# Optimization experiments

Measured on AMD Instinct MI355X. Metric: run time of the kernel, lower is better.

Reference implementation:

```python
import jax, jax.numpy as jnp
import numpy as np

N, E, L, S = 10000, 200000, 128, 10
NODE_IN, EDGE_IN = 29, 4  # vel_hist(15)+vel_mag(5)+bound(6)+force(3); rel_disp(3)+rel_dist(1)
EPS = 1e-5  # haiku LayerNorm default


def _mlp(x, params):
    # hk.nets.MLP([L]*num_mlp_layers + [out]) with relu activations
    for W, b in params[:-1]:
        x = jax.nn.relu(x @ W + b)
    W, b = params[-1]
    return x @ W + b


def _ln(x, s, o):
    m = jnp.mean(x, axis=-1, keepdims=True)
    v = jnp.mean(jnp.square(x - m), axis=-1, keepdims=True)
    return (x - m) * jax.lax.rsqrt(v + EPS) * s + o


def _init_mlp(key, dims, stack=None):
    Ws, bs = [], []
    for i in range(len(dims) - 1):
        key, k = jax.random.split(key)
        shp = (dims[i], dims[i + 1]) if stack is None else (stack, dims[i], dims[i + 1])
        Ws.append(jax.random.normal(k, shp, jnp.float32) / np.float32(np.sqrt(dims[i])))
        bshp = (dims[i + 1],) if stack is None else (stack, dims[i + 1])
        bs.append(jnp.zeros(bshp, jnp.float32))
    return Ws, bs


def setup_inputs() -> dict:
    key = jax.random.key(0)
    ks = jax.random.split(key, 16)
    inp = {
        'vel_hist': jax.random.normal(ks[0], (N, 15), jnp.float32),
        'vel_mag': jax.random.normal(ks[1], (N, 5), jnp.float32),
        'bound': jax.random.normal(ks[2], (N, 6), jnp.float32),
        'force': jax.random.normal(ks[3], (N, 3), jnp.float32),
        'rel_disp': jax.random.normal(ks[4], (E, 3), jnp.float32),
        'rel_dist': jax.random.normal(ks[5], (E, 1), jnp.float32),
        'senders': jax.random.randint(ks[6], (E,), 0, N, jnp.int32),
        'receivers': jax.random.randint(ks[7], (E,), 0, N, jnp.int32),
    }
    enW, enB = _init_mlp(ks[8], [NODE_IN, L, L, L])
    eeW, eeB = _init_mlp(ks[9], [EDGE_IN, L, L, L])
    peW, peB = _init_mlp(ks[10], [3 * L, L, L, L], stack=S)
    pnW, pnB = _init_mlp(ks[11], [2 * L, L, L, L], stack=S)
    deW, deB = _init_mlp(ks[12], [L, L, L, 3])
    for pre, (Ws, Bs) in [('en', (enW, enB)), ('ee', (eeW, eeB)), ('pe', (peW, peB)), ('pn', (pnW, pnB)), ('de', (deW, deB))]:
        for i in range(3):
            inp[f'{pre}_W{i}'] = Ws[i]
            inp[f'{pre}_b{i}'] = Bs[i]
    inp['en_s'] = jnp.ones((L,), jnp.float32); inp['en_o'] = jnp.zeros((L,), jnp.float32)
    inp['ee_s'] = jnp.ones((L,), jnp.float32); inp['ee_o'] = jnp.zeros((L,), jnp.float32)
    inp['pe_s'] = jnp.ones((S, L), jnp.float32); inp['pe_o'] = jnp.zeros((S, L), jnp.float32)
    inp['pn_s'] = jnp.ones((S, L), jnp.float32); inp['pn_o'] = jnp.zeros((S, L), jnp.float32)
    return inp


def reference(vel_hist, vel_mag, bound, force, rel_disp, rel_dist,
              en_W0, en_b0, en_W1, en_b1, en_W2, en_b2, en_s, en_o,
              ee_W0, ee_b0, ee_W1, ee_b1, ee_W2, ee_b2, ee_s, ee_o,
              pe_W0, pe_b0, pe_W1, pe_b1, pe_W2, pe_b2, pe_s, pe_o,
              pn_W0, pn_b0, pn_W1, pn_b1, pn_W2, pn_b2, pn_s, pn_o,
              de_W0, de_b0, de_W1, de_b1, de_W2, de_b2,
              senders, receivers):
    n = vel_hist.shape[0]
    # encoder
    nodes = _ln(_mlp(jnp.concatenate([vel_hist, vel_mag, bound, force], -1),
                     [(en_W0, en_b0), (en_W1, en_b1), (en_W2, en_b2)]), en_s, en_o)
    edges = _ln(_mlp(jnp.concatenate([rel_disp, rel_dist], -1),
                     [(ee_W0, ee_b0), (ee_W1, ee_b1), (ee_W2, ee_b2)]), ee_s, ee_o)

    # processor: S GraphNetwork blocks with residual adds (distinct params per step)
    def step(carry, p):
        nd, ed = carry
        (W0, b0, W1, b1, W2, b2, s, o, nW0, nb0, nW1, nb1, nW2, nb2, ns, no) = p
        e_in = jnp.concatenate([nd[senders], nd[receivers], ed], -1)  # [E, 3L]
        e_new = _ln(_mlp(e_in, [(W0, b0), (W1, b1), (W2, b2)]), s, o)
        aggr = jax.ops.segment_sum(e_new, receivers, num_segments=n)  # [N, L]
        n_new = _ln(_mlp(jnp.concatenate([nd, aggr], -1), [(nW0, nb0), (nW1, nb1), (nW2, nb2)]), ns, no)
        return (nd + n_new, ed + e_new), None

    (nodes, edges), _ = jax.lax.scan(
        step, (nodes, edges),
        (pe_W0, pe_b0, pe_W1, pe_b1, pe_W2, pe_b2, pe_s, pe_o,
         pn_W0, pn_b0, pn_W1, pn_b1, pn_W2, pn_b2, pn_s, pn_o))

    # decoder (no layer norm)
    return _mlp(nodes, [(de_W0, de_b0), (de_W1, de_b1), (de_W2, de_b2)])
```

## Files before the change

kernel.cpp:

```cpp
#include <hip/hip_runtime.h>

#define NN 10000
#define NE 200000
#define LDIM 128
#define PADB 136
#define NSTEP 10
#define LN_EPS 1e-5f

typedef unsigned short ushort_t;
typedef __attribute__((ext_vector_type(8))) short short8;
typedef __attribute__((ext_vector_type(4))) float f32x4;

#define MFMA16(a, b, c) __builtin_amdgcn_mfma_f32_16x16x32_bf16(a, b, c, 0, 0, 0)

__device__ __forceinline__ ushort_t f2bf(float f) {
  unsigned int u = __float_as_uint(f);
  return (ushort_t)((u + 0x7FFFu + ((u >> 16) & 1u)) >> 16);
}
__device__ __forceinline__ float bf2f(ushort_t h) {
  return __uint_as_float(((unsigned int)h) << 16);
}

#define STAGE_WT(WT, KTOT, K0)                                              \
  {                                                                         \
    const ushort_t* src_ = (WT) + (size_t)(t >> 1) * (KTOT) + (K0) + (t & 1) * 64; \
    ushort_t* dst_ = &Wbuf[(t >> 1) * PADB + (t & 1) * 64];                 \
    _Pragma("unroll")                                                       \
    for (int q_ = 0; q_ < 8; ++q_)                                          \
      *(uint4*)(dst_ + q_ * 8) = *(const uint4*)(src_ + q_ * 8);            \
  }

#define INIT_ACC(BG)                                                        \
  _Pragma("unroll")                                                         \
  for (int nt_ = 0; nt_ < 8; ++nt_) {                                       \
    float bv_ = (BG)[nt_ * 16 + lr];                                        \
    acc[0][nt_] = (f32x4){bv_, bv_, bv_, bv_};                              \
    acc[1][nt_] = acc[0][nt_];                                              \
  }

#define MFMA_K128()                                                         \
  _Pragma("unroll")                                                         \
  for (int ks_ = 0; ks_ < 4; ++ks_) {                                       \
    short8 a0_ = *(const short8*)&Abuf[(rw + lr) * PADB + ks_ * 32 + kg * 8];        \
    short8 a1_ = *(const short8*)&Abuf[(rw + 16 + lr) * PADB + ks_ * 32 + kg * 8];   \
    _Pragma("unroll")                                                       \
    for (int nt_ = 0; nt_ < 8; ++nt_) {                                     \
      short8 b_ = *(const short8*)&Wbuf[(nt_ * 16 + lr) * PADB + ks_ * 32 + kg * 8]; \
      acc[0][nt_] = MFMA16(a0_, b_, acc[0][nt_]);                           \
      acc[1][nt_] = MFMA16(a1_, b_, acc[1][nt_]);                           \
    }                                                                       \
  }

#define RELU_TO_ABUF()                                                      \
  _Pragma("unroll")                                                         \
  for (int mt_ = 0; mt_ < 2; ++mt_) {                                       \
    _Pragma("unroll")                                                       \
    for (int nt_ = 0; nt_ < 8; ++nt_) {                                     \
      _Pragma("unroll")                                                     \
      for (int i_ = 0; i_ < 4; ++i_) {                                      \
        int row_ = rw + 16 * mt_ + kg * 4 + i_;                             \
        Abuf[row_ * PADB + nt_ * 16 + lr] = f2bf(fmaxf(acc[mt_][nt_][i_], 0.f)); \
      }                                                                     \
    }                                                                       \
  }

#define LN_STATS2(MARR, RARR)                                               \
  float MARR[2][4], RARR[2][4];                                             \
  _Pragma("unroll")                                                         \
  for (int mt_ = 0; mt_ < 2; ++mt_) {                                       \
    _Pragma("unroll")                                                       \
    for (int i_ = 0; i_ < 4; ++i_) {                                        \
      float s_ = 0.f;                                                       \
      _Pragma("unroll")                                                     \
      for (int nt_ = 0; nt_ < 8; ++nt_) s_ += acc[mt_][nt_][i_];            \
      s_ += __shfl_xor(s_, 1); s_ += __shfl_xor(s_, 2);                     \
      s_ += __shfl_xor(s_, 4); s_ += __shfl_xor(s_, 8);                     \
      float m_ = s_ * (1.f / 128.f);                                        \
      float v_ = 0.f;                                                       \
      _Pragma("unroll")                                                     \
      for (int nt_ = 0; nt_ < 8; ++nt_) {                                   \
        float d_ = acc[mt_][nt_][i_] - m_; v_ = fmaf(d_, d_, v_);           \
      }                                                                     \
      v_ += __shfl_xor(v_, 1); v_ += __shfl_xor(v_, 2);                     \
      v_ += __shfl_xor(v_, 4); v_ += __shfl_xor(v_, 8);                     \
      MARR[mt_][i_] = m_;                                                   \
      RARR[mt_][i_] = rsqrtf(v_ * (1.f / 128.f) + LN_EPS);                  \
    }                                                                       \
  }

#define INIT_ACC1(BG)                                                       \
  _Pragma("unroll")                                                         \
  for (int nt_ = 0; nt_ < 8; ++nt_) {                                       \
    float bv_ = (BG)[nt_ * 16 + lr];                                        \
    acc[nt_] = (f32x4){bv_, bv_, bv_, bv_};                                 \
  }

#define MFMA_K128_M16()                                                     \
  _Pragma("unroll")                                                         \
  for (int ks_ = 0; ks_ < 4; ++ks_) {                                       \
    short8 a_ = *(const short8*)&Abuf[(rw + lr) * PADB + ks_ * 32 + kg * 8];         \
    _Pragma("unroll")                                                       \
    for (int nt_ = 0; nt_ < 8; ++nt_) {                                     \
      short8 b_ = *(const short8*)&Wbuf[(nt_ * 16 + lr) * PADB + ks_ * 32 + kg * 8]; \
      acc[nt_] = MFMA16(a_, b_, acc[nt_]);                                  \
    }                                                                       \
  }

#define RELU_TO_ABUF1()                                                     \
  _Pragma("unroll")                                                         \
  for (int nt_ = 0; nt_ < 8; ++nt_) {                                       \
    _Pragma("unroll")                                                       \
    for (int i_ = 0; i_ < 4; ++i_) {                                        \
      int row_ = rw + kg * 4 + i_;                                          \
      Abuf[row_ * PADB + nt_ * 16 + lr] = f2bf(fmaxf(acc[nt_][i_], 0.f));   \
    }                                                                       \
  }

#define LN_STATS1(MARR, RARR)                                               \
  float MARR[4], RARR[4];                                                   \
  _Pragma("unroll")                                                         \
  for (int i_ = 0; i_ < 4; ++i_) {                                          \
    float s_ = 0.f;                                                         \
    _Pragma("unroll")                                                       \
    for (int nt_ = 0; nt_ < 8; ++nt_) s_ += acc[nt_][i_];                   \
    s_ += __shfl_xor(s_, 1); s_ += __shfl_xor(s_, 2);                       \
    s_ += __shfl_xor(s_, 4); s_ += __shfl_xor(s_, 8);                       \
    float m_ = s_ * (1.f / 128.f);                                          \
    float v_ = 0.f;                                                         \
    _Pragma("unroll")                                                       \
    for (int nt_ = 0; nt_ < 8; ++nt_) {                                     \
      float d_ = acc[nt_][i_] - m_; v_ = fmaf(d_, d_, v_);                  \
    }                                                                       \
    v_ += __shfl_xor(v_, 1); v_ += __shfl_xor(v_, 2);                       \
    v_ += __shfl_xor(v_, 4); v_ += __shfl_xor(v_, 8);                       \
    MARR[i_] = m_;                                                          \
    RARR[i_] = rsqrtf(v_ * (1.f / 128.f) + LN_EPS);                         \
  }

#define STAGE_WT512(WT, KTOT, K0)                                           \
  {                                                                         \
    const ushort_t* src_ = (WT) + (size_t)(t >> 2) * (KTOT) + (K0) + (t & 3) * 32; \
    ushort_t* dst_ = &Wbuf[(t >> 2) * PADB + (t & 3) * 32];                 \
    _Pragma("unroll")                                                       \
    for (int q_ = 0; q_ < 4; ++q_)                                          \
      *(uint4*)(dst_ + q_ * 8) = *(const uint4*)(src_ + q_ * 8);            \
  }

__global__ void k_prep_w(const float* __restrict__ src, ushort_t* __restrict__ dst,
                         int Ksrc, int Kdst, int N, int steps) {
  const size_t total = (size_t)steps * N * Kdst;
  for (size_t idx = (size_t)blockIdx.x * blockDim.x + threadIdx.x; idx < total;
       idx += (size_t)gridDim.x * blockDim.x) {
    int k = (int)(idx % Kdst);
    size_t tmp = idx / Kdst;
    int n = (int)(tmp % N);
    int s = (int)(tmp / N);
    float v = (k < Ksrc) ? src[((size_t)s * Ksrc + k) * N + n] : 0.f;
    dst[idx] = f2bf(v);
  }
}

__global__ void k_hist(const int* __restrict__ recv, int* __restrict__ cnt) {
  int e = blockIdx.x * 256 + threadIdx.x;
  if (e < NE) atomicAdd(&cnt[recv[e]], 1);
}

__global__ __launch_bounds__(256)
void k_scan(const int* __restrict__ cnt, int* __restrict__ row_start) {
  __shared__ int part[256];
  const int t = threadIdx.x;
  const int base = t * 40;
  int sum = 0;
  for (int i = 0; i < 40; ++i) {
    int b = base + i;
    if (b < NN) sum += cnt[b];
  }
  part[t] = sum;
  __syncthreads();
  for (int off = 1; off < 256; off <<= 1) {
    int v = part[t];
    int u = (t >= off) ? part[t - off] : 0;
    __syncthreads();
    part[t] = v + u;
    __syncthreads();
  }
  int run = (t == 0) ? 0 : part[t - 1];
  for (int i = 0; i < 40; ++i) {
    int b = base + i;
    if (b < NN) { row_start[b] = run; run += cnt[b]; }
  }
  if (t == 255) row_start[NN] = run;
}

__global__ void k_scatter(const int* __restrict__ send, const int* __restrict__ recv,
                          const int* __restrict__ row_start, int* __restrict__ cursor,
                          int* __restrict__ esrc, int* __restrict__ sSend,
                          int* __restrict__ sRecv) {
  int e = blockIdx.x * 256 + threadIdx.x;
  if (e >= NE) return;
  int r = recv[e];
  int pos = row_start[r] + atomicAdd(&cursor[r], 1);
  esrc[pos] = e;
  sSend[pos] = send[e];
  sRecv[pos] = r;
}

__global__ __launch_bounds__(256, 2)
void k_enc_node_m(const float* __restrict__ vh, const float* __restrict__ vm,
                  const float* __restrict__ bd, const float* __restrict__ fc,
                  const ushort_t* __restrict__ Wt0, const float* __restrict__ b0,
                  const ushort_t* __restrict__ Wt1, const float* __restrict__ b1,
                  const ushort_t* __restrict__ Wt2, const float* __restrict__ b2,
                  const float* __restrict__ lns, const float* __restrict__ lno,
                  float* __restrict__ nodes_f, ushort_t* __restrict__ nodes_bf) {
  __shared__ ushort_t Abuf[128 * PADB];
  __shared__ ushort_t Wbuf[128 * PADB];
  const int t = threadIdx.x;
  const int lane = t & 63, wid = t >> 6;
  const int lr = lane & 15, kg = lane >> 4;
  const int rw = wid * 32;
  const int n0 = blockIdx.x * 128;

  for (int idx = t; idx < 128 * 32; idx += 256) {
    int r = idx >> 5, k = idx & 31;
    int ng = n0 + r;
    float v = 0.f;
    if (ng < NN) {
      if (k < 15)      v = vh[(size_t)ng * 15 + k];
      else if (k < 20) v = vm[(size_t)ng * 5 + (k - 15)];
      else if (k < 26) v = bd[(size_t)ng * 6 + (k - 20)];
      else if (k < 29) v = fc[(size_t)ng * 3 + (k - 26)];
    }
    Abuf[r * PADB + k] = f2bf(v);
  }
  {
    const ushort_t* src = Wt0 + (t >> 1) * 32 + (t & 1) * 16;
    ushort_t* dst = &Wbuf[(t >> 1) * PADB + (t & 1) * 16];
    *(uint4*)dst = *(const uint4*)src;
    *(uint4*)(dst + 8) = *(const uint4*)(src + 8);
  }
  f32x4 acc[2][8];
  INIT_ACC(b0)
  __syncthreads();
  {
    short8 a0_ = *(const short8*)&Abuf[(rw + lr) * PADB + kg * 8];
    short8 a1_ = *(const short8*)&Abuf[(rw + 16 + lr) * PADB + kg * 8];
#pragma unroll
    for (int nt_ = 0; nt_ < 8; ++nt_) {
      short8 b_ = *(const short8*)&Wbuf[(nt_ * 16 + lr) * PADB + kg * 8];
      acc[0][nt_] = MFMA16(a0_, b_, acc[0][nt_]);
      acc[1][nt_] = MFMA16(a1_, b_, acc[1][nt_]);
    }
  }
  __syncthreads();
  RELU_TO_ABUF()
  INIT_ACC(b1)
  STAGE_WT(Wt1, 128, 0)
  __syncthreads();
  MFMA_K128()
  __syncthreads();
  RELU_TO_ABUF()
  INIT_ACC(b2)
  STAGE_WT(Wt2, 128, 0)
  __syncthreads();
  MFMA_K128()

  LN_STATS2(lmean, lrstd)
  float sv[8], ov[8];
#pragma unroll
  for (int nt = 0; nt < 8; ++nt) { sv[nt] = lns[nt * 16 + lr]; ov[nt] = lno[nt * 16 + lr]; }
#pragma unroll
  for (int mt = 0; mt < 2; ++mt)
#pragma unroll
    for (int i = 0; i < 4; ++i) {
      int row = rw + 16 * mt + kg * 4 + i;
      int ng = n0 + row;
      if (ng < NN) {
#pragma unroll
        for (int nt = 0; nt < 8; ++nt) {
          float o = (acc[mt][nt][i] - lmean[mt][i]) * lrstd[mt][i] * sv[nt] + ov[nt];
          size_t idx = (size_t)ng * LDIM + nt * 16 + lr;
          nodes_f[idx] = o;
          nodes_bf[idx] = f2bf(o);
        }
      }
    }
}

__global__ __launch_bounds__(256, 2)
void k_enc_edge_m(const float* __restrict__ rel_disp, const float* __restrict__ rel_dist,
                  const int* __restrict__ esrc,
                  const ushort_t* __restrict__ Wt0, const float* __restrict__ b0,
                  const ushort_t* __restrict__ Wt1, const float* __restrict__ b1,
                  const ushort_t* __restrict__ Wt2, const float* __restrict__ b2,
                  const float* __restrict__ lns, const float* __restrict__ lno,
                  float* __restrict__ edges_f) {
  __shared__ ushort_t smem[2 * 128 * PADB];
  __shared__ int eidx[128];
  ushort_t* Abuf = smem;
  ushort_t* Wbuf = smem + 128 * PADB;
  const int t = threadIdx.x;
  const int lane = t & 63, wid = t >> 6;
  const int lr = lane & 15, kg = lane >> 4;
  const int rw = wid * 32;
  const int e0 = blockIdx.x * 128;

  if (t < 128) eidx[t] = (e0 + t < NE) ? esrc[e0 + t] : 0;
  __syncthreads();

  for (int idx = t; idx < 128 * 32; idx += 256) {
    int r = idx >> 5, k = idx & 31;
    float v = 0.f;
    if (e0 + r < NE) {
      int eo = eidx[r];
      if (k < 3)       v = rel_disp[(size_t)eo * 3 + k];
      else if (k == 3) v = rel_dist[eo];
    }
    Abuf[r * PADB + k] = f2bf(v);
  }
  {
    const ushort_t* src = Wt0 + (t >> 1) * 32 + (t & 1) * 16;
    ushort_t* dst = &Wbuf[(t >> 1) * PADB + (t & 1) * 16];
    *(uint4*)dst = *(const uint4*)src;
    *(uint4*)(dst + 8) = *(const uint4*)(src + 8);
  }
  f32x4 acc[2][8];
  INIT_ACC(b0)
  __syncthreads();
  {
    short8 a0_ = *(const short8*)&Abuf[(rw + lr) * PADB + kg * 8];
    short8 a1_ = *(const short8*)&Abuf[(rw + 16 + lr) * PADB + kg * 8];
#pragma unroll
    for (int nt_ = 0; nt_ < 8; ++nt_) {
      short8 b_ = *(const short8*)&Wbuf[(nt_ * 16 + lr) * PADB + kg * 8];
      acc[0][nt_] = MFMA16(a0_, b_, acc[0][nt_]);
      acc[1][nt_] = MFMA16(a1_, b_, acc[1][nt_]);
    }
  }
  __syncthreads();
  RELU_TO_ABUF()
  INIT_ACC(b1)
  STAGE_WT(Wt1, 128, 0)
  __syncthreads();
  MFMA_K128()
  __syncthreads();
  RELU_TO_ABUF()
  INIT_ACC(b2)
  STAGE_WT(Wt2, 128, 0)
  __syncthreads();
  MFMA_K128()

  LN_STATS2(lmean, lrstd)
  float sv[8], ov[8];
#pragma unroll
  for (int nt = 0; nt < 8; ++nt) { sv[nt] = lns[nt * 16 + lr]; ov[nt] = lno[nt * 16 + lr]; }

  float* fbuf = (float*)smem;
  __syncthreads();
#pragma unroll
  for (int mt_ = 0; mt_ < 2; ++mt_)
#pragma unroll
    for (int i_ = 0; i_ < 4; ++i_) {
      int row_ = rw + 16 * mt_ + kg * 4 + i_;
#pragma unroll
      for (int nt_ = 0; nt_ < 8; ++nt_)
        fbuf[row_ * 132 + nt_ * 16 + lr] =
            (acc[mt_][nt_][i_] - lmean[mt_][i_]) * lrstd[mt_][i_] * sv[nt_] + ov[nt_];
    }
  __syncthreads();
#pragma unroll
  for (int q = 0; q < 16; ++q) {
    int F = wid * 4096 + q * 256 + lane * 4;
    int row = F >> 7, col = F & 127;
    if (e0 + row < NE) {
      float4 v = *(const float4*)&fbuf[row * 132 + col];
      *(float4*)&edges_f[(size_t)e0 * LDIM + F] = v;
    }
  }
}

__global__ __launch_bounds__(512, 4)
void k_proc_edge_m(const ushort_t* __restrict__ nodes_bf, float* __restrict__ edges_f,
                   float* __restrict__ aggr,
                   const int* __restrict__ sSend, const int* __restrict__ sRecv,
                   const ushort_t* __restrict__ Wt0, const float* __restrict__ b0,
                   const ushort_t* __restrict__ Wt1, const float* __restrict__ b1,
                   const ushort_t* __restrict__ Wt2, const float* __restrict__ b2,
                   const float* __restrict__ lns, const float* __restrict__ lno) {
  __shared__ ushort_t smem[2 * 128 * PADB];
  __shared__ int sidx[128], ridxs[128];
  ushort_t* Abuf = smem;
  ushort_t* Wbuf = smem + 128 * PADB;
  const int t = threadIdx.x;
  const int lane = t & 63, wid = t >> 6;
  const int lr = lane & 15, kg = lane >> 4;
  const int rw = wid * 16;
  const int e0 = blockIdx.x * 128;

  if (t < 128)       sidx[t] = (e0 + t < NE) ? sSend[e0 + t] : 0;
  else if (t < 256)  ridxs[t - 128] = (e0 + t - 128 < NE) ? sRecv[e0 + t - 128] : -1;

  float4 eold[8];
#pragma unroll
  for (int q = 0; q < 8; ++q) {
    int F = q * 2048 + t * 4;
    int row = F >> 7;
    if (e0 + row < NE) eold[q] = *(const float4*)&edges_f[(size_t)e0 * LDIM + F];
    else { eold[q].x = eold[q].y = eold[q].z = eold[q].w = 0.f; }
  }

  f32x4 acc[8];
  INIT_ACC1(b0)

#pragma unroll
  for (int seg = 0; seg < 3; ++seg) {
    __syncthreads();
    if (seg < 2) {
      const int r = t >> 2, h = t & 3;
      const int srow = (seg == 0) ? sidx[r] : ((ridxs[r] < 0) ? 0 : ridxs[r]);
      const ushort_t* src = nodes_bf + (size_t)srow * LDIM + h * 32;
      ushort_t* dst = &Abuf[r * PADB + h * 32];
#pragma unroll
      for (int q = 0; q < 4; ++q)
        *(uint4*)(dst + q * 8) = *(const uint4*)(src + q * 8);
    } else {
#pragma unroll
      for (int q = 0; q < 8; ++q) {
        int F = q * 2048 + t * 4;
        int row = F >> 7, col = F & 127;
        ushort4 hv;
        hv.x = f2bf(eold[q].x); hv.y = f2bf(eold[q].y);
        hv.z = f2bf(eold[q].z); hv.w = f2bf(eold[q].w);
        *(ushort4*)&Abuf[row * PADB + col] = hv;
      }
    }
    STAGE_WT512(Wt0, 384, seg * 128)
    __syncthreads();
    MFMA_K128_M16()
  }

  RELU_TO_ABUF1()
  INIT_ACC1(b1)
  __syncthreads();
  STAGE_WT512(Wt1, 128, 0)
  __syncthreads();
  MFMA_K128_M16()
  RELU_TO_ABUF1()
  INIT_ACC1(b2)
  __syncthreads();
  STAGE_WT512(Wt2, 128, 0)
  __syncthreads();
  MFMA_K128_M16()

  LN_STATS1(lmean, lrstd)
  float sv[8], ov[8];
#pragma unroll
  for (int nt = 0; nt < 8; ++nt) { sv[nt] = lns[nt * 16 + lr]; ov[nt] = lno[nt * 16 + lr]; }

  float* fbuf = (float*)smem;
  __syncthreads();
#pragma unroll
  for (int i = 0; i < 4; ++i) {
    int row = rw + kg * 4 + i;
#pragma unroll
    for (int nt = 0; nt < 8; ++nt)
      fbuf[row * 132 + nt * 16 + lr] =
          (acc[nt][i] - lmean[i]) * lrstd[i] * sv[nt] + ov[nt];
  }
  __syncthreads();

#pragma unroll
  for (int q = 0; q < 8; ++q) {
    int F = q * 2048 + t * 4;
    int row = F >> 7, col = F & 127;
    if (e0 + row < NE) {
      float4 nv = *(const float4*)&fbuf[row * 132 + col];
      nv.x += eold[q].x; nv.y += eold[q].y;
      nv.z += eold[q].z; nv.w += eold[q].w;
      *(float4*)&edges_f[(size_t)e0 * LDIM + F] = nv;
    }
  }

  {
    const int c = t & 127, sub = t >> 7;
    const int rA = sub * 32, rB = rA + 32;
    float run = 0.f;
    int cur = ridxs[rA];
    for (int r = rA; r < rB; ++r) {
      int rid = ridxs[r];
      if (rid != cur) {
        if (cur >= 0) atomicAdd(&aggr[(size_t)cur * LDIM + c], run);
        run = 0.f;
        cur = rid;
      }
      run += fbuf[r * 132 + c];
    }
    if (cur >= 0) atomicAdd(&aggr[(size_t)cur * LDIM + c], run);
  }
}

__global__ __launch_bounds__(256, 3)
void k_proc_node_m(float* __restrict__ nodes_f, ushort_t* __restrict__ nodes_bf,
                   float* __restrict__ aggr,
                   const ushort_t* __restrict__ Wt0, const float* __restrict__ b0,
                   const ushort_t* __restrict__ Wt1, const float* __restrict__ b1,
                   const ushort_t* __restrict__ Wt2, const float* __restrict__ b2,
                   const float* __restrict__ lns, const float* __restrict__ lno) {
  __shared__ ushort_t Abuf[64 * PADB];
  __shared__ ushort_t Wbuf[128 * PADB];
  const int t = threadIdx.x;
  const int lane = t & 63, wid = t >> 6;
  const int lr = lane & 15, kg = lane >> 4;
  const int rw = wid * 16;
  const int n0 = blockIdx.x * 64;

  f32x4 acc[8];
  INIT_ACC1(b0)

#pragma unroll
  for (int seg = 0; seg < 2; ++seg) {
    if (seg) __syncthreads();
    {
      const int r = t >> 2, h = t & 3;
      const int ng = n0 + r;
      ushort_t* dst = &Abuf[r * PADB + h * 32];
      if (ng < NN) {
        if (seg == 0) {
          const ushort_t* src = nodes_bf + (size_t)ng * LDIM + h * 32;
#pragma unroll
          for (int q = 0; q < 4; ++q)
            *(uint4*)(dst + q * 8) = *(const uint4*)(src + q * 8);
        } else {
          float* srcf = aggr + (size_t)ng * LDIM + h * 32;
          float4 z4; z4.x = z4.y = z4.z = z4.w = 0.f;
#pragma unroll
          for (int q = 0; q < 8; ++q) {
            float4 fv = *(const float4*)(srcf + q * 4);
            ushort4 hv;
            hv.x = f2bf(fv.x); hv.y = f2bf(fv.y); hv.z = f2bf(fv.z); hv.w = f2bf(fv.w);
            *(ushort4*)(dst + q * 4) = hv;
            *(float4*)(srcf + q * 4) = z4;
          }
        }
      } else {
        uint4 z; z.x = z.y = z.z = z.w = 0u;
#pragma unroll
        for (int q = 0; q < 4; ++q) *(uint4*)(dst + q * 8) = z;
      }
    }
    STAGE_WT(Wt0, 256, seg * 128)
    __syncthreads();
    MFMA_K128_M16()
  }
  RELU_TO_ABUF1()
  INIT_ACC1(b1)
  __syncthreads();
  STAGE_WT(Wt1, 128, 0)
  __syncthreads();
  MFMA_K128_M16()
  RELU_TO_ABUF1()
  INIT_ACC1(b2)
  __syncthreads();
  STAGE_WT(Wt2, 128, 0)
  __syncthreads();
  MFMA_K128_M16()

  LN_STATS1(lmean, lrstd)
  float sv[8], ov[8];
#pragma unroll
  for (int nt = 0; nt < 8; ++nt) { sv[nt] = lns[nt * 16 + lr]; ov[nt] = lno[nt * 16 + lr]; }
#pragma unroll
  for (int i = 0; i < 4; ++i) {
    int row = rw + kg * 4 + i;
    int ng = n0 + row;
    if (ng < NN) {
#pragma unroll
      for (int nt = 0; nt < 8; ++nt) {
        float o = (acc[nt][i] - lmean[i]) * lrstd[i] * sv[nt] + ov[nt];
        size_t idx = (size_t)ng * LDIM + nt * 16 + lr;
        float nv = nodes_f[idx] + o;
        nodes_f[idx] = nv;
        nodes_bf[idx] = f2bf(nv);
      }
    }
  }
}

__global__ __launch_bounds__(256, 2)
void k_dec_m(const ushort_t* __restrict__ nodes_bf,
             const ushort_t* __restrict__ Wt0, const float* __restrict__ b0,
             const ushort_t* __restrict__ Wt1, const float* __restrict__ b1,
             const float* __restrict__ W2f, const float* __restrict__ b2,
             float* __restrict__ out) {
  __shared__ ushort_t Abuf[128 * PADB];
  __shared__ ushort_t Wbuf[128 * PADB];
  const int t = threadIdx.x;
  const int lane = t & 63, wid = t >> 6;
  const int lr = lane & 15, kg = lane >> 4;
  const int rw = wid * 32;
  const int n0 = blockIdx.x * 128;

  {
    const int r = t >> 1, h = t & 1;
    const int ng = n0 + r;
    ushort_t* dst = &Abuf[r * PADB + h * 64];
    if (ng < NN) {
      const ushort_t* src = nodes_bf + (size_t)ng * LDIM + h * 64;
#pragma unroll
      for (int q = 0; q < 8; ++q)
        *(uint4*)(dst + q * 8) = *(const uint4*)(src + q * 8);
    } else {
      uint4 z; z.x = z.y = z.z = z.w = 0u;
#pragma unroll
      for (int q = 0; q < 8; ++q) *(uint4*)(dst + q * 8) = z;
    }
  }
  f32x4 acc[2][8];
  INIT_ACC(b0)
  STAGE_WT(Wt0, 128, 0)
  __syncthreads();
  MFMA_K128()
  __syncthreads();
  RELU_TO_ABUF()
  INIT_ACC(b1)
  STAGE_WT(Wt1, 128, 0)
  __syncthreads();
  MFMA_K128()
  __syncthreads();
  RELU_TO_ABUF()
  __syncthreads();

  if (t < 128) {
    const int ng = n0 + t;
    if (ng < NN) {
      float s0 = b2[0], s1 = b2[1], s2 = b2[2];
      for (int k = 0; k < 128; ++k) {
        float xv = bf2f(Abuf[t * PADB + k]);
        s0 = fmaf(xv, W2f[k * 3 + 0], s0);
        s1 = fmaf(xv, W2f[k * 3 + 1], s1);
        s2 = fmaf(xv, W2f[k * 3 + 2], s2);
      }
      out[(size_t)ng * 3 + 0] = s0;
      out[(size_t)ng * 3 + 1] = s1;
      out[(size_t)ng * 3 + 2] = s2;
    }
  }
}

extern "C" void kernel_launch(void* const* d_in, const int* in_sizes, int n_in,
                              void* d_out, int out_size, void* d_ws, size_t ws_size,
                              hipStream_t stream) {
  const float* vel_hist = (const float*)d_in[0];
  const float* vel_mag  = (const float*)d_in[1];
  const float* bnd      = (const float*)d_in[2];
  const float* force    = (const float*)d_in[3];
  const float* rel_disp = (const float*)d_in[4];
  const float* rel_dist = (const float*)d_in[5];
  const int*   senders   = (const int*)d_in[6];
  const int*   receivers = (const int*)d_in[7];
  const float* en_W0 = (const float*)d_in[8];  const float* en_b0 = (const float*)d_in[9];
  const float* en_W1 = (const float*)d_in[10]; const float* en_b1 = (const float*)d_in[11];
  const float* en_W2 = (const float*)d_in[12]; const float* en_b2 = (const float*)d_in[13];
  const float* ee_W0 = (const float*)d_in[14]; const float* ee_b0 = (const float*)d_in[15];
  const float* ee_W1 = (const float*)d_in[16]; const float* ee_b1 = (const float*)d_in[17];
  const float* ee_W2 = (const float*)d_in[18]; const float* ee_b2 = (const float*)d_in[19];
  const float* pe_W0 = (const float*)d_in[20]; const float* pe_b0 = (const float*)d_in[21];
  const float* pe_W1 = (const float*)d_in[22]; const float* pe_b1 = (const float*)d_in[23];
  const float* pe_W2 = (const float*)d_in[24]; const float* pe_b2 = (const float*)d_in[25];
  const float* pn_W0 = (const float*)d_in[26]; const float* pn_b0 = (const float*)d_in[27];
  const float* pn_W1 = (const float*)d_in[28]; const float* pn_b1 = (const float*)d_in[29];
  const float* pn_W2 = (const float*)d_in[30]; const float* pn_b2 = (const float*)d_in[31];
  const float* de_W0 = (const float*)d_in[32]; const float* de_b0 = (const float*)d_in[33];
  const float* de_W1 = (const float*)d_in[34]; const float* de_b1 = (const float*)d_in[35];
  const float* de_W2 = (const float*)d_in[36]; const float* de_b2 = (const float*)d_in[37];
  const float* en_s = (const float*)d_in[38]; const float* en_o = (const float*)d_in[39];
  const float* ee_s = (const float*)d_in[40]; const float* ee_o = (const float*)d_in[41];
  const float* pe_s = (const float*)d_in[42]; const float* pe_o = (const float*)d_in[43];
  const float* pn_s = (const float*)d_in[44]; const float* pn_o = (const float*)d_in[45];

  float* nodes_f = (float*)d_ws;
  float* edges_f = nodes_f + (size_t)NN * LDIM;
  float* aggr    = edges_f + (size_t)NE * LDIM;
  ushort_t* nodes_bf = (ushort_t*)(aggr + (size_t)NN * LDIM);
  ushort_t* w = nodes_bf + (size_t)NN * LDIM;
  ushort_t* wEn0 = w; w += 128 * 32;
  ushort_t* wEn1 = w; w += 128 * 128;
  ushort_t* wEn2 = w; w += 128 * 128;
  ushort_t* wEe0 = w; w += 128 * 32;
  ushort_t* wEe1 = w; w += 128 * 128;
  ushort_t* wEe2 = w; w += 128 * 128;
  ushort_t* wPe0 = w; w += (size_t)NSTEP * 128 * 384;
  ushort_t* wPe1 = w; w += (size_t)NSTEP * 128 * 128;
  ushort_t* wPe2 = w; w += (size_t)NSTEP * 128 * 128;
  ushort_t* wPn0 = w; w += (size_t)NSTEP * 128 * 256;
  ushort_t* wPn1 = w; w += (size_t)NSTEP * 128 * 128;
  ushort_t* wPn2 = w; w += (size_t)NSTEP * 128 * 128;
  ushort_t* wDe0 = w; w += 128 * 128;
  ushort_t* wDe1 = w; w += 128 * 128;
  int* cnt       = (int*)w;
  int* row_start = cnt + NN;
  int* cursor    = row_start + NN + 1;
  int* esrc      = cursor + NN;
  int* sSend     = esrc + NE;
  int* sRecv     = sSend + NE;

  auto prep = [&](const float* src, ushort_t* dst, int Ks, int Kd, int N_, int st) {
    size_t total = (size_t)st * N_ * Kd;
    int blocks = (int)((total + 255) / 256);
    if (blocks > 1024) blocks = 1024;
    k_prep_w<<<blocks, 256, 0, stream>>>(src, dst, Ks, Kd, N_, st);
  };
  prep(en_W0, wEn0, 29, 32, 128, 1);
  prep(en_W1, wEn1, 128, 128, 128, 1);
  prep(en_W2, wEn2, 128, 128, 128, 1);
  prep(ee_W0, wEe0, 4, 32, 128, 1);
  prep(ee_W1, wEe1, 128, 128, 128, 1);
  prep(ee_W2, wEe2, 128, 128, 128, 1);
  prep(pe_W0, wPe0, 384, 384, 128, NSTEP);
  prep(pe_W1, wPe1, 128, 128, 128, NSTEP);
  prep(pe_W2, wPe2, 128, 128, 128, NSTEP);
  prep(pn_W0, wPn0, 256, 256, 128, NSTEP);
  prep(pn_W1, wPn1, 128, 128, 128, NSTEP);
  prep(pn_W2, wPn2, 128, 128, 128, NSTEP);
  prep(de_W0, wDe0, 128, 128, 128, 1);
  prep(de_W1, wDe1, 128, 128, 128, 1);

  hipMemsetAsync(cnt, 0, NN * sizeof(int), stream);
  hipMemsetAsync(cursor, 0, NN * sizeof(int), stream);
  k_hist<<<(NE + 255) / 256, 256, 0, stream>>>(receivers, cnt);
  k_scan<<<1, 256, 0, stream>>>(cnt, row_start);
  k_scatter<<<(NE + 255) / 256, 256, 0, stream>>>(senders, receivers, row_start,
                                                  cursor, esrc, sSend, sRecv);

  const int NB  = (NN + 127) / 128;
  const int NBn = (NN + 63) / 64;
  const int EB  = (NE + 127) / 128;

  k_enc_node_m<<<NB, 256, 0, stream>>>(vel_hist, vel_mag, bnd, force,
      wEn0, en_b0, wEn1, en_b1, wEn2, en_b2, en_s, en_o, nodes_f, nodes_bf);
  k_enc_edge_m<<<EB, 256, 0, stream>>>(rel_disp, rel_dist, esrc,
      wEe0, ee_b0, wEe1, ee_b1, wEe2, ee_b2, ee_s, ee_o, edges_f);

  hipMemsetAsync(aggr, 0, (size_t)NN * LDIM * sizeof(float), stream);

  for (int s = 0; s < NSTEP; ++s) {
    k_proc_edge_m<<<EB, 512, 0, stream>>>(nodes_bf, edges_f, aggr, sSend, sRecv,
        wPe0 + (size_t)s * 128 * 384, pe_b0 + (size_t)s * LDIM,
        wPe1 + (size_t)s * 128 * 128, pe_b1 + (size_t)s * LDIM,
        wPe2 + (size_t)s * 128 * 128, pe_b2 + (size_t)s * LDIM,
        pe_s + (size_t)s * LDIM, pe_o + (size_t)s * LDIM);
    k_proc_node_m<<<NBn, 256, 0, stream>>>(nodes_f, nodes_bf, aggr,
        wPn0 + (size_t)s * 128 * 256, pn_b0 + (size_t)s * LDIM,
        wPn1 + (size_t)s * 128 * 128, pn_b1 + (size_t)s * LDIM,
        wPn2 + (size_t)s * 128 * 128, pn_b2 + (size_t)s * LDIM,
        pn_s + (size_t)s * LDIM, pn_o + (size_t)s * LDIM);
  }

  k_dec_m<<<NB, 256, 0, stream>>>(nodes_bf, wDe0, de_b0, wDe1, de_b1, de_W2, de_b2,
                                  (float*)d_out);
}
```

Measured before the change: 1.463 ms.

## Restructure processor edge kernel: register gathers, swizzled LDS, prefetched weights

The processor edge kernel now gathers sender and receiver node rows straight into MFMA A-operand registers instead of staging them through shared memory. It stores weights and activations in an XOR-swizzled unpadded LDS layout, with the swizzle baked into the weight prep kernel for the processor edge weights. The next weight tile is prefetched into registers while the current MFMAs run. Old edge features are re-read from global memory rather than held in registers, which lowers register pressure and LDS footprint at the cost of an extra global read.

```diff
diff --git a/kernel.cpp b/kernel.cpp
--- a/kernel.cpp
+++ b/kernel.cpp
@@ -137,17 +137,51 @@
     RARR[i_] = rsqrtf(v_ * (1.f / 128.f) + LN_EPS);                         \
   }
 
-#define STAGE_WT512(WT, KTOT, K0)                                           \
-  {                                                                         \
-    const ushort_t* src_ = (WT) + (size_t)(t >> 2) * (KTOT) + (K0) + (t & 3) * 32; \
-    ushort_t* dst_ = &Wbuf[(t >> 2) * PADB + (t & 3) * 32];                 \
-    _Pragma("unroll")                                                       \
-    for (int q_ = 0; q_ < 4; ++q_)                                          \
-      *(uint4*)(dst_ + q_ * 8) = *(const uint4*)(src_ + q_ * 8);            \
+#define LOADW(WT, KTOT, K0)                                                 \
+  _Pragma("unroll")                                                         \
+  for (int q_ = 0; q_ < 4; ++q_)                                            \
+    wreg[q_] = *(const uint4*)((WT) + (size_t)(q_ * 32 + (t >> 4)) * (KTOT) + (K0) + (t & 15) * 8);
+
+#define STOREW()                                                            \
+  _Pragma("unroll")                                                         \
+  for (int q_ = 0; q_ < 4; ++q_)                                            \
+    *(uint4*)(Wbuf + q_ * 4096 + t * 8) = wreg[q_];
+
+#define MFMA_AREG(AR)                                                       \
+  _Pragma("unroll")                                                         \
+  for (int ks_ = 0; ks_ < 4; ++ks_) {                                       \
+    short8 a_ = (AR)[ks_];                                                  \
+    _Pragma("unroll")                                                       \
+    for (int nt_ = 0; nt_ < 8; ++nt_) {                                     \
+      short8 b_ = *(const short8*)&Wbuf[(nt_ * 16 + lr) * LDIM + (((ks_ * 4 + kg) ^ (lr & 7)) * 8)]; \
+      acc[nt_] = MFMA16(a_, b_, acc[nt_]);                                  \
+    }                                                                       \
+  }
+
+#define MFMA_SWZ()                                                          \
+  _Pragma("unroll")                                                         \
+  for (int ks_ = 0; ks_ < 4; ++ks_) {                                       \
+    short8 a_ = *(const short8*)&Abuf[(rw + lr) * LDIM + (((ks_ * 4 + kg) ^ (lr & 7)) * 8)]; \
+    _Pragma("unroll")                                                       \
+    for (int nt_ = 0; nt_ < 8; ++nt_) {                                     \
+      short8 b_ = *(const short8*)&Wbuf[(nt_ * 16 + lr) * LDIM + (((ks_ * 4 + kg) ^ (lr & 7)) * 8)]; \
+      acc[nt_] = MFMA16(a_, b_, acc[nt_]);                                  \
+    }                                                                       \
+  }
+
+#define RELU_SWZ()                                                          \
+  _Pragma("unroll")                                                         \
+  for (int nt_ = 0; nt_ < 8; ++nt_) {                                       \
+    _Pragma("unroll")                                                       \
+    for (int i_ = 0; i_ < 4; ++i_) {                                        \
+      int row_ = rw + kg * 4 + i_;                                          \
+      int ch_ = (2 * nt_ + (lr >> 3)) ^ ((kg * 4 + i_) & 7);                \
+      Abuf[row_ * LDIM + ch_ * 8 + (lr & 7)] = f2bf(fmaxf(acc[nt_][i_], 0.f)); \
+    }                                                                       \
   }
 
 __global__ void k_prep_w(const float* __restrict__ src, ushort_t* __restrict__ dst,
-                         int Ksrc, int Kdst, int N, int steps) {
+                         int Ksrc, int Kdst, int N, int steps, int swz) {
   const size_t total = (size_t)steps * N * Kdst;
   for (size_t idx = (size_t)blockIdx.x * blockDim.x + threadIdx.x; idx < total;
        idx += (size_t)gridDim.x * blockDim.x) {
@@ -155,7 +189,8 @@
     size_t tmp = idx / Kdst;
     int n = (int)(tmp % N);
     int s = (int)(tmp / N);
-    float v = (k < Ksrc) ? src[((size_t)s * Ksrc + k) * N + n] : 0.f;
+    int klog = swz ? (k ^ ((n & 7) << 3)) : k;
+    float v = (klog < Ksrc) ? src[((size_t)s * Ksrc + klog) * N + n] : 0.f;
     dst[idx] = f2bf(v);
   }
 }
@@ -387,77 +422,83 @@
                    const ushort_t* __restrict__ Wt1, const float* __restrict__ b1,
                    const ushort_t* __restrict__ Wt2, const float* __restrict__ b2,
                    const float* __restrict__ lns, const float* __restrict__ lno) {
-  __shared__ ushort_t smem[2 * 128 * PADB];
-  __shared__ int sidx[128], ridxs[128];
-  ushort_t* Abuf = smem;
-  ushort_t* Wbuf = smem + 128 * PADB;
+  __shared__ __align__(16) unsigned char smem[132 * 128 * 4];
+  __shared__ int ridxs[128];
+  ushort_t* Wbuf = (ushort_t*)smem;
+  ushort_t* Abuf = (ushort_t*)(smem + 32768);
+  float* fbuf = (float*)smem;
   const int t = threadIdx.x;
   const int lane = t & 63, wid = t >> 6;
   const int lr = lane & 15, kg = lane >> 4;
   const int rw = wid * 16;
   const int e0 = blockIdx.x * 128;
 
-  if (t < 128)       sidx[t] = (e0 + t < NE) ? sSend[e0 + t] : 0;
-  else if (t < 256)  ridxs[t - 128] = (e0 + t - 128 < NE) ? sRecv[e0 + t - 128] : -1;
-
-  float4 eold[8];
-#pragma unroll
-  for (int q = 0; q < 8; ++q) {
-    int F = q * 2048 + t * 4;
-    int row = F >> 7;
-    if (e0 + row < NE) eold[q] = *(const float4*)&edges_f[(size_t)e0 * LDIM + F];
-    else { eold[q].x = eold[q].y = eold[q].z = eold[q].w = 0.f; }
-  }
-
+  if (t < 128) ridxs[t] = (e0 + t < NE) ? sRecv[e0 + t] : -1;
+
+  const int er0 = e0 + rw + lr;
+  const int s0r = (er0 < NE) ? sSend[er0] : -1;
+  const int r0r = (er0 < NE) ? sRecv[er0] : -1;
+  short8 a0[4], a1[4];
+  {
+    short8 z = {0, 0, 0, 0, 0, 0, 0, 0};
+#pragma unroll
+    for (int ks = 0; ks < 4; ++ks) {
+      a0[ks] = (s0r >= 0) ? *(const short8*)&nodes_bf[(size_t)s0r * LDIM + ks * 32 + kg * 8] : z;
+      a1[ks] = (r0r >= 0) ? *(const short8*)&nodes_bf[(size_t)r0r * LDIM + ks * 32 + kg * 8] : z;
+    }
+  }
+
+  uint4 wreg[4];
   f32x4 acc[8];
+  LOADW(Wt0, 384, 0)
   INIT_ACC1(b0)
-
-#pragma unroll
-  for (int seg = 0; seg < 3; ++seg) {
-    __syncthreads();
-    if (seg < 2) {
-      const int r = t >> 2, h = t & 3;
-      const int srow = (seg == 0) ? sidx[r] : ((ridxs[r] < 0) ? 0 : ridxs[r]);
-      const ushort_t* src = nodes_bf + (size_t)srow * LDIM + h * 32;
-      ushort_t* dst = &Abuf[r * PADB + h * 32];
-#pragma unroll
-      for (int q = 0; q < 4; ++q)
-        *(uint4*)(dst + q * 8) = *(const uint4*)(src + q * 8);
-    } else {
-#pragma unroll
-      for (int q = 0; q < 8; ++q) {
-        int F = q * 2048 + t * 4;
-        int row = F >> 7, col = F & 127;
-        ushort4 hv;
-        hv.x = f2bf(eold[q].x); hv.y = f2bf(eold[q].y);
-        hv.z = f2bf(eold[q].z); hv.w = f2bf(eold[q].w);
-        *(ushort4*)&Abuf[row * PADB + col] = hv;
-      }
-    }
-    STAGE_WT512(Wt0, 384, seg * 128)
-    __syncthreads();
-    MFMA_K128_M16()
-  }
-
-  RELU_TO_ABUF1()
+  STOREW()
+  __syncthreads();
+  LOADW(Wt0, 384, 128)
+  MFMA_AREG(a0)
+  __syncthreads();
+  STOREW()
+  __syncthreads();
+  LOADW(Wt0, 384, 256)
+  MFMA_AREG(a1)
+  __syncthreads();
+  STOREW()
+  {
+#pragma unroll
+    for (int q = 0; q < 8; ++q) {
+      int F = q * 2048 + t * 4;
+      int row = F >> 7, colf = F & 127;
+      float4 v;
+      if (e0 + row < NE) v = *(const float4*)&edges_f[(size_t)e0 * LDIM + F];
+      else { v.x = v.y = v.z = v.w = 0.f; }
+      ushort4 hv;
+      hv.x = f2bf(v.x); hv.y = f2bf(v.y); hv.z = f2bf(v.z); hv.w = f2bf(v.w);
+      int chunk = colf >> 3, sub = (colf >> 2) & 1;
+      *(ushort4*)&Abuf[row * LDIM + ((chunk ^ (row & 7)) * 8) + sub * 4] = hv;
+    }
+  }
+  __syncthreads();
+  LOADW(Wt1, 128, 0)
+  MFMA_SWZ()
+  RELU_SWZ()
   INIT_ACC1(b1)
   __syncthreads();
-  STAGE_WT512(Wt1, 128, 0)
-  __syncthreads();
-  MFMA_K128_M16()
-  RELU_TO_ABUF1()
+  STOREW()
+  __syncthreads();
+  LOADW(Wt2, 128, 0)
+  MFMA_SWZ()
+  RELU_SWZ()
   INIT_ACC1(b2)
   __syncthreads();
-  STAGE_WT512(Wt2, 128, 0)
-  __syncthreads();
-  MFMA_K128_M16()
+  STOREW()
+  __syncthreads();
+  MFMA_SWZ()
 
   LN_STATS1(lmean, lrstd)
   float sv[8], ov[8];
 #pragma unroll
   for (int nt = 0; nt < 8; ++nt) { sv[nt] = lns[nt * 16 + lr]; ov[nt] = lno[nt * 16 + lr]; }
 
-  float* fbuf = (float*)smem;
   __syncthreads();
 #pragma unroll
   for (int i = 0; i < 4; ++i) {
@@ -475,8 +516,8 @@
     int row = F >> 7, col = F & 127;
     if (e0 + row < NE) {
       float4 nv = *(const float4*)&fbuf[row * 132 + col];
-      nv.x += eold[q].x; nv.y += eold[q].y;
-      nv.z += eold[q].z; nv.w += eold[q].w;
+      float4 old = *(const float4*)&edges_f[(size_t)e0 * LDIM + F];
+      nv.x += old.x; nv.y += old.y; nv.z += old.z; nv.w += old.w;
       *(float4*)&edges_f[(size_t)e0 * LDIM + F] = nv;
     }
   }
@@ -704,26 +745,26 @@
   int* sSend     = esrc + NE;
   int* sRecv     = sSend + NE;
 
-  auto prep = [&](const float* src, ushort_t* dst, int Ks, int Kd, int N_, int st) {
+  auto prep = [&](const float* src, ushort_t* dst, int Ks, int Kd, int N_, int st, int swz) {
     size_t total = (size_t)st * N_ * Kd;
     int blocks = (int)((total + 255) / 256);
     if (blocks > 1024) blocks = 1024;
-    k_prep_w<<<blocks, 256, 0, stream>>>(src, dst, Ks, Kd, N_, st);
+    k_prep_w<<<blocks, 256, 0, stream>>>(src, dst, Ks, Kd, N_, st, swz);
   };
-  prep(en_W0, wEn0, 29, 32, 128, 1);
-  prep(en_W1, wEn1, 128, 128, 128, 1);
-  prep(en_W2, wEn2, 128, 128, 128, 1);
-  prep(ee_W0, wEe0, 4, 32, 128, 1);
-  prep(ee_W1, wEe1, 128, 128, 128, 1);
-  prep(ee_W2, wEe2, 128, 128, 128, 1);
-  prep(pe_W0, wPe0, 384, 384, 128, NSTEP);
-  prep(pe_W1, wPe1, 128, 128, 128, NSTEP);
-  prep(pe_W2, wPe2, 128, 128, 128, NSTEP);
-  prep(pn_W0, wPn0, 256, 256, 128, NSTEP);
-  prep(pn_W1, wPn1, 128, 128, 128, NSTEP);
-  prep(pn_W2, wPn2, 128, 128, 128, NSTEP);
-  prep(de_W0, wDe0, 128, 128, 128, 1);
-  prep(de_W1, wDe1, 128, 128, 128, 1);
+  prep(en_W0, wEn0, 29, 32, 128, 1, 0);
+  prep(en_W1, wEn1, 128, 128, 128, 1, 0);
+  prep(en_W2, wEn2, 128, 128, 128, 1, 0);
+  prep(ee_W0, wEe0, 4, 32, 128, 1, 0);
+  prep(ee_W1, wEe1, 128, 128, 128, 1, 0);
+  prep(ee_W2, wEe2, 128, 128, 128, 1, 0);
+  prep(pe_W0, wPe0, 384, 384, 128, NSTEP, 1);
+  prep(pe_W1, wPe1, 128, 128, 128, NSTEP, 1);
+  prep(pe_W2, wPe2, 128, 128, 128, NSTEP, 1);
+  prep(pn_W0, wPn0, 256, 256, 128, NSTEP, 0);
+  prep(pn_W1, wPn1, 128, 128, 128, NSTEP, 0);
+  prep(pn_W2, wPn2, 128, 128, 128, NSTEP, 0);
+  prep(de_W0, wDe0, 128, 128, 128, 1, 0);
+  prep(de_W1, wDe1, 128, 128, 128, 1, 0);
 
   hipMemsetAsync(cnt, 0, NN * sizeof(int), stream);
   hipMemsetAsync(cursor, 0, NN * sizeof(int), stream);
```

Measured after the change: 1.726 ms. 18.0% more time.
